# Performance work log

Measured on AMD Instinct MI355X. Metric: run time of the kernel, lower is better.

Reference implementation:

```python
import jax, jax.numpy as jnp
import numpy as np

# Model dims (match init_kwargs)
N_HEADS = 32
N_KV_HEADS = 8
DIM = 4096
HEAD_DIM = DIM // N_HEADS  # 128
N_REP = N_HEADS // N_KV_HEADS  # 4
MAX_SEQ_LEN = 2048
THETA = 10000.0


def precompute_freqs(dim, end, theta=THETA):
    inv = 1.0 / (theta ** (jnp.arange(0, dim, 2, dtype=jnp.float32) / dim))  # [dim/2]
    t = jnp.arange(end, dtype=jnp.float32)
    f = jnp.outer(t, inv)  # [end, dim/2]
    return jnp.cos(f), jnp.sin(f)


def apply_rope(x, cos, sin):
    # x: [b, s, h, d]; cos/sin: [s, d/2]. Pairs (x[...,2i], x[...,2i+1]) form complex numbers.
    xr = x[..., 0::2]
    xi = x[..., 1::2]
    c = cos[None, :, None, :]
    s = sin[None, :, None, :]
    out_r = xr * c - xi * s
    out_i = xr * s + xi * c
    return jnp.stack([out_r, out_i], axis=-1).reshape(x.shape)


def setup_inputs() -> dict:
    key = jax.random.key(0)
    ks = jax.random.split(key, 5)
    B, S = 4, 1024
    x = jax.random.normal(ks[0], (B, S, DIM), dtype=jnp.float32)
    wq = jax.random.normal(ks[1], (DIM, N_HEADS * HEAD_DIM), dtype=jnp.float32) * 0.02
    wk = jax.random.normal(ks[2], (DIM, N_KV_HEADS * HEAD_DIM), dtype=jnp.float32) * 0.02
    wv = jax.random.normal(ks[3], (DIM, N_KV_HEADS * HEAD_DIM), dtype=jnp.float32) * 0.02
    wo = jax.random.normal(ks[4], (N_HEADS * HEAD_DIM, DIM), dtype=jnp.float32) * 0.02
    # causal mask, additive: 0 on/below diagonal, -1e9 above
    mask = jnp.where(jnp.tril(jnp.ones((S, S), dtype=bool)), 0.0, -1e9).astype(jnp.float32)[None, None]
    return {"x": x, "wq": wq, "wk": wk, "wv": wv, "wo": wo, "mask": mask, "start_pos": 0}


def reference(x, wq, wk, wv, wo, mask, start_pos):
    B, S, _ = x.shape
    # QKV projections
    xq = (x @ wq).reshape(B, S, N_HEADS, HEAD_DIM)
    xk = (x @ wk).reshape(B, S, N_KV_HEADS, HEAD_DIM)
    xv = (x @ wv).reshape(B, S, N_KV_HEADS, HEAD_DIM)
    # RoPE on q, k at positions [start_pos, start_pos+S)
    cos, sin = precompute_freqs(HEAD_DIM, MAX_SEQ_LEN * 2)
    cos_s = jax.lax.dynamic_slice_in_dim(cos, start_pos, S, 0)
    sin_s = jax.lax.dynamic_slice_in_dim(sin, start_pos, S, 0)
    xq = apply_rope(xq, cos_s, sin_s)
    xk = apply_rope(xk, cos_s, sin_s)
    # KV-cache scatter-update (cache starts zeroed), then read prefix
    cache_k = jnp.zeros((B, MAX_SEQ_LEN, N_KV_HEADS, HEAD_DIM), dtype=x.dtype)
    cache_v = jnp.zeros_like(cache_k)
    cache_k = jax.lax.dynamic_update_slice(cache_k, xk, (0, start_pos, 0, 0))
    cache_v = jax.lax.dynamic_update_slice(cache_v, xv, (0, start_pos, 0, 0))
    kv_len = start_pos + S
    keys = cache_k[:, :kv_len]    # [b, kv_len, n_kv, d]
    values = cache_v[:, :kv_len]
    # GQA without materializing repeated KV: split q heads into (kv_group, rep)
    q = xq.reshape(B, S, N_KV_HEADS, N_REP, HEAD_DIM)
    scale = 1.0 / jnp.sqrt(jnp.float32(HEAD_DIM)).astype(x.dtype)
    scores = jnp.einsum('bsgrd,btgd->bgrst', q, keys) * scale  # [b, g, r, s, t]
    scores = scores + mask.reshape(1, 1, 1, S, kv_len)
    probs = jax.nn.softmax(scores, axis=-1)
    out = jnp.einsum('bgrst,btgd->bsgrd', probs, values)  # [b, s, g, r, d]
    out = out.reshape(B, S, N_HEADS * HEAD_DIM)
    return out @ wo
```

## Files before the change

kernel.cpp:

```cpp
#include <hip/hip_runtime.h>
#include <hip/hip_bf16.h>
#include <stdint.h>

typedef __bf16 bf16raw;
typedef __attribute__((ext_vector_type(8))) __bf16 bf16x8;
typedef __attribute__((ext_vector_type(4))) float f32x4;

#define DIMD 4096
#define NHEAD 32
#define NKVH 8
#define HD 128
#define SEQ 1024
#define NB 4
#define NTOK 4096
#define NQKV 6144

__device__ __forceinline__ void gload_lds16(const void* gsrc, void* ldst) {
  __builtin_amdgcn_global_load_lds(
      (const __attribute__((address_space(1))) void*)gsrc,
      (__attribute__((address_space(3))) void*)ldst, 16, 0, 0);
}

__global__ void cast_f32_bf16_kernel(const float* __restrict__ src,
                                     __hip_bfloat16* __restrict__ dst, int n) {
  int i = (blockIdx.x * 256 + threadIdx.x) * 8;
  if (i >= n) return;
  f32x4 a = *(const f32x4*)(src + i);
  f32x4 b = *(const f32x4*)(src + i + 4);
  union { bf16x8 v; __hip_bfloat16 e[8]; } o;
#pragma unroll
  for (int j = 0; j < 4; ++j) {
    o.e[j] = __float2bfloat16(a[j]);
    o.e[4 + j] = __float2bfloat16(b[j]);
  }
  *(bf16x8*)(dst + i) = o.v;
}

__global__ void transpose_qkv_kernel(const float* __restrict__ wq,
                                     const float* __restrict__ wk,
                                     const float* __restrict__ wv,
                                     __hip_bfloat16* __restrict__ dst) {
  __shared__ float tile[32][33];
  int n0 = blockIdx.x * 32;
  int k0 = blockIdx.y * 32;
  const float* src;
  int scol, nsw;
  if (n0 < 4096) { src = wq; scol = n0; nsw = 4096; }
  else if (n0 < 5120) { src = wk; scol = n0 - 4096; nsw = 1024; }
  else { src = wv; scol = n0 - 5120; nsw = 1024; }
  int tx = threadIdx.x, ty = threadIdx.y;
#pragma unroll
  for (int i = 0; i < 4; ++i)
    tile[ty + 8 * i][tx] = src[(size_t)(k0 + ty + 8 * i) * nsw + scol + tx];
  __syncthreads();
  union { ushort4 u; __hip_bfloat16 e[4]; } pk;
#pragma unroll
  for (int jj = 0; jj < 4; ++jj)
    pk.e[jj] = __float2bfloat16(tile[ty * 4 + jj][tx]);
  *(ushort4*)(dst + (size_t)(n0 + tx) * 4096 + k0 + ty * 4) = pk.u;
}

__global__ void transpose_wo_kernel(const float* __restrict__ src,
                                    __hip_bfloat16* __restrict__ dst) {
  __shared__ float tile[32][33];
  int n0 = blockIdx.x * 32, k0 = blockIdx.y * 32;
  int tx = threadIdx.x, ty = threadIdx.y;
#pragma unroll
  for (int i = 0; i < 4; ++i)
    tile[ty + 8 * i][tx] = src[(size_t)(k0 + ty + 8 * i) * 4096 + n0 + tx];
  __syncthreads();
  union { ushort4 u; __hip_bfloat16 e[4]; } pk;
#pragma unroll
  for (int jj = 0; jj < 4; ++jj)
    pk.e[jj] = __float2bfloat16(tile[ty * 4 + jj][tx]);
  *(ushort4*)(dst + (size_t)(n0 + tx) * 4096 + k0 + ty * 4) = pk.u;
}

__global__ void rope_table_kernel(float* __restrict__ cosb, float* __restrict__ sinb) {
  int idx = blockIdx.x * 256 + threadIdx.x;
  int s = idx >> 6, j = idx & 63;
  float inv = 1.0f / powf(10000.0f, (float)(2 * j) * (1.0f / 128.0f));
  float ang = (float)s * inv;
  cosb[idx] = cosf(ang);
  sinb[idx] = sinf(ang);
}


#define LGSB()                                       \
  asm volatile("s_waitcnt lgkmcnt(0)" ::: "memory"); \
  __builtin_amdgcn_sched_barrier(0)

#define QMFMA(AFR, BFR, MB, NB)                                            \
  _Pragma("unroll") for (int mf2 = 0; mf2 < 4; ++mf2)                      \
  _Pragma("unroll") for (int nf2 = 0; nf2 < 2; ++nf2)                      \
  _Pragma("unroll") for (int kk2 = 0; kk2 < 2; ++kk2)                      \
      acc[(MB) + mf2][(NB) + nf2] = __builtin_amdgcn_mfma_f32_16x16x32_bf16( \
          AFR[mf2 * 2 + kk2], BFR[nf2 * 2 + kk2], acc[(MB) + mf2][(NB) + nf2], 0, 0, 0)

#define TILE4(BUF, ST1, ST2, ST3, ST4, VM)                        \
  {                                                               \
    _Pragma("unroll") for (int mf = 0; mf < 4; ++mf)              \
    _Pragma("unroll") for (int kk = 0; kk < 2; ++kk)              \
        alo[mf * 2 + kk] = ldsA(BUF, mf, kk);                     \
    _Pragma("unroll") for (int nf = 0; nf < 2; ++nf)              \
    _Pragma("unroll") for (int kk = 0; kk < 2; ++kk)              \
        bq[nf * 2 + kk] = ldsB(BUF, nf, kk);                      \
    ST1;                                                          \
    LGSB();                                                       \
    __builtin_amdgcn_s_setprio(1);                                \
    QMFMA(alo, bq, 0, 0);                                         \
    __builtin_amdgcn_s_setprio(0);                                \
    _Pragma("unroll") for (int mf = 0; mf < 4; ++mf)              \
    _Pragma("unroll") for (int kk = 0; kk < 2; ++kk)              \
        ahi[mf * 2 + kk] = ldsA(BUF, mf + 4, kk);                 \
    ST2;                                                          \
    LGSB();                                                       \
    __builtin_amdgcn_s_setprio(1);                                \
    QMFMA(ahi, bq, 4, 0);                                         \
    __builtin_amdgcn_s_setprio(0);                                \
    _Pragma("unroll") for (int nf = 0; nf < 2; ++nf)              \
    _Pragma("unroll") for (int kk = 0; kk < 2; ++kk)              \
        bq[nf * 2 + kk] = ldsB(BUF, nf + 2, kk);                  \
    LGSB();                                                       \
    __builtin_amdgcn_s_setprio(1);                                \
    QMFMA(alo, bq, 0, 2);                                         \
    __builtin_amdgcn_s_setprio(0);                                \
    __builtin_amdgcn_s_barrier();   \
    ST3;                                                          \
    ST4;                                                          \
    __builtin_amdgcn_s_setprio(1);                                \
    QMFMA(ahi, bq, 4, 2);                                         \
    __builtin_amdgcn_s_setprio(0);                                \
    VM;                                                           \
    __builtin_amdgcn_s_barrier();   \
  }

template <typename OutT, bool ROPE>
__global__ __launch_bounds__(512, 2) void gemm256_kernel(
    const __hip_bfloat16* __restrict__ A, const __hip_bfloat16* __restrict__ BT,
    OutT* __restrict__ C, int M, int N, int K,
    const float* __restrict__ cosb, const float* __restrict__ sinb,
    __hip_bfloat16* __restrict__ vtc) {
  __shared__ __align__(16) char lds_[131072];
  const int tid = threadIdx.x;
  const int w = tid >> 6, l = tid & 63;
  const int lr = l & 15, lk = l >> 4;
  const int wm = w >> 2, wn = w & 3;

  const int nbn = N >> 8;
  const int nwg = (M >> 8) * nbn;
  const int cpx = nwg >> 3;
  const int bid = blockIdx.x;
  const int swz = (bid & 7) * cpx + (bid >> 3);
  const int m0 = (swz / nbn) << 8;
  const int n0 = (swz % nbn) << 8;

  const size_t Kb = (size_t)K * 2;
  const char* Ab = (const char*)A + (size_t)m0 * Kb;
  const char* Bb = (const char*)BT + (size_t)n0 * Kb;
  const int srcb = ((l & 7) ^ (l >> 3)) * 16;
  const int crow = l >> 3;

  auto stageA = [&](int buf, int half, int kt) {
#pragma unroll
    for (int j = 0; j < 2; ++j) {
      int row = half * 128 + (w * 2 + j) * 8 + crow;
      gload_lds16(Ab + (size_t)row * Kb + (size_t)kt * 128 + srcb,
                  lds_ + buf * 65536 + half * 16384 + (w * 2 + j) * 1024);
    }
  };
  auto stageB = [&](int buf, int half, int kt) {
#pragma unroll
    for (int j = 0; j < 2; ++j) {
      int row = half * 128 + (w * 2 + j) * 8 + crow;
      gload_lds16(Bb + (size_t)row * Kb + (size_t)kt * 128 + srcb,
                  lds_ + buf * 65536 + 32768 + half * 16384 + (w * 2 + j) * 1024);
    }
  };
  auto ldsA = [&](int buf, int mf, int kk) {
    int rih = mf * 16 + lr;
    int cb = (kk * 64 + lk * 16) ^ ((lr & 7) << 4);
    return *(const bf16x8*)(lds_ + buf * 65536 + wm * 16384 + rih * 128 + cb);
  };
  auto ldsB = [&](int buf, int nf, int kk) {
    int rih = (wn & 1) * 64 + nf * 16 + lr;
    int cb = (kk * 64 + lk * 16) ^ ((lr & 7) << 4);
    return *(const bf16x8*)(lds_ + buf * 65536 + 32768 + (wn >> 1) * 16384 +
                            rih * 128 + cb);
  };

  f32x4 acc[8][4] = {};
  bf16x8 alo[8], ahi[8], bq[4];

  stageA(0, 0, 0);
  stageA(0, 1, 0);
  stageB(0, 0, 0);
  stageB(0, 1, 0);
  stageA(1, 0, 1);
  stageA(1, 1, 1);
  asm volatile("s_waitcnt vmcnt(4)" ::: "memory");
  __builtin_amdgcn_s_barrier();

  const int NT = K >> 6;
  for (int E = 0; E < NT - 2; E += 2) {
    TILE4(0, stageB(1, 0, E + 1), stageB(1, 1, E + 1),
          stageA(0, 0, E + 2), stageA(0, 1, E + 2),
          asm volatile("s_waitcnt vmcnt(4)" ::: "memory"));
    TILE4(1, stageB(0, 0, E + 2), stageB(0, 1, E + 2),
          stageA(1, 0, E + 3), stageA(1, 1, E + 3),
          asm volatile("s_waitcnt vmcnt(4)" ::: "memory"));
  }
  TILE4(0, stageB(1, 0, NT - 1), stageB(1, 1, NT - 1), (void)0, (void)0,
        asm volatile("s_waitcnt vmcnt(0)" ::: "memory"));
  TILE4(1, (void)0, (void)0, (void)0, (void)0, (void)0);

#pragma unroll
  for (int mf = 0; mf < 8; ++mf) {
    int row = m0 + wm * 128 + mf * 16 + lk * 4;
#pragma unroll
    for (int nf = 0; nf < 4; ++nf) {
      int colb = n0 + wn * 64 + nf * 16;
      f32x4 v = acc[mf][nf];
      if constexpr (ROPE) {
        if (colb < 5120) {
          int d = (colb & 127) + lr;
          int jj = d >> 1;
          bool even = (d & 1) == 0;
#pragma unroll
          for (int j = 0; j < 4; ++j) {
            float p = __shfl_xor(v[j], 1);
            int s = (row + j) & (SEQ - 1);
            float c = cosb[s * 64 + jj];
            float sn = sinb[s * 64 + jj];
            v[j] = even ? (v[j] * c - p * sn) : (p * sn + v[j] * c);
          }
        } else {
          int col = colb + lr;
          int d = col & 127;
          int hk = (col >> 7) & 7;
          int b = row >> 10;
          int s = row & (SEQ - 1);
          union { uint64_t u; __hip_bfloat16 e[4]; } pk;
#pragma unroll
          for (int j = 0; j < 4; ++j) pk.e[j] = __float2bfloat16(v[j]);
          size_t off = ((size_t)((b * 8 + hk) * 16 + (s >> 6)) * 128 + d) * 64 +
                       (s & 63);
          *(uint64_t*)(vtc + off) = pk.u;
          continue;
        }
      }
#pragma unroll
      for (int j = 0; j < 4; ++j) {
        size_t off = (size_t)(row + j) * N + colb + lr;
        if constexpr (sizeof(OutT) == 2)
          C[off] = __float2bfloat16(v[j]);
        else
          C[off] = v[j];
      }
    }
  }
}

__global__ __launch_bounds__(512, 2) void attn_kernel(
    const __hip_bfloat16* __restrict__ qkv,
    const __hip_bfloat16* __restrict__ vtc,
    __hip_bfloat16* __restrict__ out) {
  __shared__ __align__(16) char Ks[2][16384];
  __shared__ __align__(16) char Vs[2][16384];
  __shared__ __align__(16) char Ps[8][4096];

  const int tid = threadIdx.x;
  const int w = tid >> 6, l = tid & 63;
  const int lr = l & 15, lk = l >> 4;
  const int bx = blockIdx.x;
  const int p = bx >> 5;
  const int bh = bx & 31;
  const int b = bh >> 3;
  const int hk = bh & 7;
  const int h = hk * 4 + (w & 3);
  const int qh = w >> 2;

  const char* KgB = (const char*)qkv +
                    ((size_t)(b * SEQ) * NQKV + DIMD + hk * HD) * 2;
  const char* VgB = (const char*)vtc + (size_t)(b * NKVH + hk) * (16 * 16384);
  char* Pw = &Ps[w][0];

  const float cs = 0.12752039889171495f;
  const float ebias = 11.541560327111707f;

  auto stageK = [&](int buf, int kvb) {
#pragma unroll
    for (int j = 0; j < 2; ++j) {
      int i2 = w * 2 + j;
      int row = i2 * 4 + (l >> 4);
      int si = ((l & 15) * 16) ^ ((row & 7) << 4);
      gload_lds16(KgB + (size_t)(kvb + row) * (NQKV * 2) + si,
                  &Ks[buf][i2 * 1024]);
    }
  };
  auto stageV = [&](int buf, int t) {
#pragma unroll
    for (int j = 0; j < 2; ++j) {
      int i2 = w * 2 + j;
      int row = i2 * 8 + (l >> 3);
      int si = ((l & 7) * 16) ^ ((row & 7) << 4);
      gload_lds16(VgB + (size_t)t * 16384 + row * 128 + si,
                  &Vs[buf][i2 * 1024]);
    }
  };

  for (int qsel = 0; qsel < 2; ++qsel) {
    const int qtile = qsel ? (15 - p) : p;
    const int qbaseW = qtile * 64 + qh * 32;
    const int nkv = qtile + 1;

    bf16x8 aq[8];
#pragma unroll
    for (int qg = 0; qg < 2; ++qg) {
      const __hip_bfloat16* Qp =
          qkv + (size_t)(b * SEQ + qbaseW + qg * 16 + lr) * NQKV + h * HD + lk * 8;
#pragma unroll
      for (int ks = 0; ks < 4; ++ks) aq[qg * 4 + ks] = *(const bf16x8*)(Qp + ks * 32);
    }

    f32x4 O[16] = {};
    float lsum[8] = {0.f, 0.f, 0.f, 0.f, 0.f, 0.f, 0.f, 0.f};

    stageK(0, 0);
    stageV(0, 0);
    asm volatile("s_waitcnt vmcnt(0)" ::: "memory");
    __syncthreads();

    for (int t = 0; t < nkv; ++t) {
      const int cur = t & 1;
      if (t + 1 < nkv) {
        stageK(cur ^ 1, (t + 1) * 64);
        stageV(cur ^ 1, t + 1);
      }
      const int kvb = t * 64;

      f32x4 st[8] = {};
      __builtin_amdgcn_s_setprio(1);
#pragma unroll
      for (int nt = 0; nt < 4; ++nt) {
        int row = nt * 16 + lr;
        const char* kr = &Ks[cur][row * 256];
        int sw = (row & 7) << 4;
        bf16x8 bk[4];
#pragma unroll
        for (int ks = 0; ks < 4; ++ks)
          bk[ks] = *(const bf16x8*)(kr + ((ks * 64 + lk * 16) ^ sw));
#pragma unroll
        for (int qg = 0; qg < 2; ++qg)
#pragma unroll
          for (int ks = 0; ks < 4; ++ks)
            st[qg * 4 + nt] = __builtin_amdgcn_mfma_f32_16x16x32_bf16(
                aq[qg * 4 + ks], bk[ks], st[qg * 4 + nt], 0, 0, 0);
      }
      __builtin_amdgcn_s_setprio(0);

#pragma unroll
      for (int qg = 0; qg < 2; ++qg) {
        const bool needmask = (kvb + 63 > qbaseW + qg * 16);
#pragma unroll
        for (int j = 0; j < 4; ++j) {
          int qrow = qbaseW + qg * 16 + lk * 4 + j;
          int prow = lk * 4 + j;
          int sw = (prow & 7) << 4;
#pragma unroll
          for (int nt = 0; nt < 4; ++nt) {
            float pv = exp2f(fmaf(st[qg * 4 + nt][j], cs, -ebias));
            if (needmask && (kvb + nt * 16 + lr > qrow)) pv = 0.f;
            lsum[qg * 4 + j] += pv;
            *(__hip_bfloat16*)(Pw + qg * 2048 + prow * 128 +
                               (((nt * 16 + lr) * 2) ^ sw)) = __float2bfloat16(pv);
          }
        }
      }

      asm volatile("s_waitcnt lgkmcnt(0)" ::: "memory");
      __builtin_amdgcn_sched_barrier(0);

      __builtin_amdgcn_s_setprio(1);
#pragma unroll
      for (int ks = 0; ks < 2; ++ks) {
        bf16x8 ap[2];
#pragma unroll
        for (int qg = 0; qg < 2; ++qg)
          ap[qg] = *(const bf16x8*)(Pw + qg * 2048 + lr * 128 +
                                    ((ks * 64 + lk * 16) ^ ((lr & 7) << 4)));
#pragma unroll
        for (int dt = 0; dt < 8; ++dt) {
          int row = dt * 16 + lr;
          bf16x8 bv = *(const bf16x8*)(&Vs[cur][row * 128 +
                                               ((ks * 64 + lk * 16) ^ ((row & 7) << 4))]);
#pragma unroll
          for (int qg = 0; qg < 2; ++qg)
            O[qg * 8 + dt] = __builtin_amdgcn_mfma_f32_16x16x32_bf16(
                ap[qg], bv, O[qg * 8 + dt], 0, 0, 0);
        }
      }
      __builtin_amdgcn_s_setprio(0);

      __syncthreads();
    }

#pragma unroll
    for (int qg = 0; qg < 2; ++qg) {
#pragma unroll
      for (int j = 0; j < 4; ++j) {
        float rs = lsum[qg * 4 + j];
        rs += __shfl_xor(rs, 1);
        rs += __shfl_xor(rs, 2);
        rs += __shfl_xor(rs, 4);
        rs += __shfl_xor(rs, 8);
        float inv = 1.0f / rs;
        __hip_bfloat16* orow =
            out + (size_t)(b * SEQ + qbaseW + qg * 16 + lk * 4 + j) * DIMD + h * HD;
#pragma unroll
        for (int dt = 0; dt < 8; ++dt)
          orow[dt * 16 + lr] = __float2bfloat16(O[qg * 8 + dt][j] * inv);
      }
    }
  }
}

extern "C" void kernel_launch(void* const* d_in, const int* in_sizes, int n_in,
                              void* d_out, int out_size, void* d_ws, size_t ws_size,
                              hipStream_t stream) {
  const float* x = (const float*)d_in[0];
  const float* wq = (const float*)d_in[1];
  const float* wk = (const float*)d_in[2];
  const float* wv = (const float*)d_in[3];
  const float* wo = (const float*)d_in[4];
  float* out = (float*)d_out;

  char* ws = (char*)d_ws;
  const size_t MB = 1024 * 1024;
  __hip_bfloat16* xb = (__hip_bfloat16*)(ws);
  __hip_bfloat16* wqkvt = (__hip_bfloat16*)(ws + 32 * MB);
  __hip_bfloat16* wot = (__hip_bfloat16*)(ws + 80 * MB);
  __hip_bfloat16* qkv = (__hip_bfloat16*)(ws + 112 * MB);
  __hip_bfloat16* vtc = (__hip_bfloat16*)(ws + 160 * MB);
  float* cosb = (float*)(ws + 168 * MB);
  float* sinb = cosb + SEQ * 64;

  cast_f32_bf16_kernel<<<NTOK * DIMD / 8 / 256, 256, 0, stream>>>(x, xb, NTOK * DIMD);
  transpose_qkv_kernel<<<dim3(192, 128), dim3(32, 8), 0, stream>>>(wq, wk, wv, wqkvt);
  transpose_wo_kernel<<<dim3(128, 128), dim3(32, 8), 0, stream>>>(wo, wot);
  rope_table_kernel<<<SEQ * 64 / 256, 256, 0, stream>>>(cosb, sinb);
  gemm256_kernel<__hip_bfloat16, true><<<dim3(384), 512, 0, stream>>>(
      xb, wqkvt, qkv, NTOK, NQKV, DIMD, cosb, sinb, vtc);
  attn_kernel<<<dim3(256), 512, 0, stream>>>(qkv, vtc, xb);
  gemm256_kernel<float, false><<<dim3(256), 512, 0, stream>>>(
      xb, wot, out, NTOK, DIMD, DIMD, nullptr, nullptr, nullptr);
}
```

Baseline: 468.7 us.

## Simplify GEMM pipeline to plain double buffering with full-tile prefetch

Replaces the staggered A/B staging schedule (A prefetched two tiles ahead, B one tile ahead, split across four points inside the tile) with simple double buffering. Each step now issues the whole next A and B tile at the start of the compute step, then waits for all loads (vmcnt(0)) before a single barrier. This cuts a barrier per tile and simplifies scheduling. The cost is a shallower prefetch and an exposed full drain of outstanding loads each iteration, so memory latency may be hidden less well.

```diff
diff --git a/kernel.cpp b/kernel.cpp
--- a/kernel.cpp
+++ b/kernel.cpp
@@ -97,15 +97,15 @@
       acc[(MB) + mf2][(NB) + nf2] = __builtin_amdgcn_mfma_f32_16x16x32_bf16( \
           AFR[mf2 * 2 + kk2], BFR[nf2 * 2 + kk2], acc[(MB) + mf2][(NB) + nf2], 0, 0, 0)
 
-#define TILE4(BUF, ST1, ST2, ST3, ST4, VM)                        \
+#define TILE1(BUF, ST)                                            \
   {                                                               \
+    ST;                                                           \
     _Pragma("unroll") for (int mf = 0; mf < 4; ++mf)              \
     _Pragma("unroll") for (int kk = 0; kk < 2; ++kk)              \
         alo[mf * 2 + kk] = ldsA(BUF, mf, kk);                     \
     _Pragma("unroll") for (int nf = 0; nf < 2; ++nf)              \
     _Pragma("unroll") for (int kk = 0; kk < 2; ++kk)              \
         bq[nf * 2 + kk] = ldsB(BUF, nf, kk);                      \
-    ST1;                                                          \
     LGSB();                                                       \
     __builtin_amdgcn_s_setprio(1);                                \
     QMFMA(alo, bq, 0, 0);                                         \
@@ -113,7 +113,6 @@
     _Pragma("unroll") for (int mf = 0; mf < 4; ++mf)              \
     _Pragma("unroll") for (int kk = 0; kk < 2; ++kk)              \
         ahi[mf * 2 + kk] = ldsA(BUF, mf + 4, kk);                 \
-    ST2;                                                          \
     LGSB();                                                       \
     __builtin_amdgcn_s_setprio(1);                                \
     QMFMA(ahi, bq, 4, 0);                                         \
@@ -125,14 +124,11 @@
     __builtin_amdgcn_s_setprio(1);                                \
     QMFMA(alo, bq, 0, 2);                                         \
     __builtin_amdgcn_s_setprio(0);                                \
-    __builtin_amdgcn_s_barrier();   \
-    ST3;                                                          \
-    ST4;                                                          \
     __builtin_amdgcn_s_setprio(1);                                \
     QMFMA(ahi, bq, 4, 2);                                         \
     __builtin_amdgcn_s_setprio(0);                                \
-    VM;                                                           \
-    __builtin_amdgcn_s_barrier();   \
+    asm volatile("s_waitcnt vmcnt(0)" ::: "memory");              \
+    __builtin_amdgcn_s_barrier();    \
   }
 
 template <typename OutT, bool ROPE>
@@ -161,21 +157,25 @@
   const int srcb = ((l & 7) ^ (l >> 3)) * 16;
   const int crow = l >> 3;
 
-  auto stageA = [&](int buf, int half, int kt) {
-#pragma unroll
-    for (int j = 0; j < 2; ++j) {
-      int row = half * 128 + (w * 2 + j) * 8 + crow;
-      gload_lds16(Ab + (size_t)row * Kb + (size_t)kt * 128 + srcb,
-                  lds_ + buf * 65536 + half * 16384 + (w * 2 + j) * 1024);
-    }
-  };
-  auto stageB = [&](int buf, int half, int kt) {
-#pragma unroll
-    for (int j = 0; j < 2; ++j) {
-      int row = half * 128 + (w * 2 + j) * 8 + crow;
-      gload_lds16(Bb + (size_t)row * Kb + (size_t)kt * 128 + srcb,
-                  lds_ + buf * 65536 + 32768 + half * 16384 + (w * 2 + j) * 1024);
-    }
+  auto stageA = [&](int buf, int kt) {
+#pragma unroll
+    for (int hf = 0; hf < 2; ++hf)
+#pragma unroll
+      for (int j = 0; j < 2; ++j) {
+        int row = hf * 128 + (w * 2 + j) * 8 + crow;
+        gload_lds16(Ab + (size_t)row * Kb + (size_t)kt * 128 + srcb,
+                    lds_ + buf * 65536 + hf * 16384 + (w * 2 + j) * 1024);
+      }
+  };
+  auto stageB = [&](int buf, int kt) {
+#pragma unroll
+    for (int hf = 0; hf < 2; ++hf)
+#pragma unroll
+      for (int j = 0; j < 2; ++j) {
+        int row = hf * 128 + (w * 2 + j) * 8 + crow;
+        gload_lds16(Bb + (size_t)row * Kb + (size_t)kt * 128 + srcb,
+                    lds_ + buf * 65536 + 32768 + hf * 16384 + (w * 2 + j) * 1024);
+      }
   };
   auto ldsA = [&](int buf, int mf, int kk) {
     int rih = mf * 16 + lr;
@@ -192,27 +192,18 @@
   f32x4 acc[8][4] = {};
   bf16x8 alo[8], ahi[8], bq[4];
 
-  stageA(0, 0, 0);
-  stageA(0, 1, 0);
-  stageB(0, 0, 0);
-  stageB(0, 1, 0);
-  stageA(1, 0, 1);
-  stageA(1, 1, 1);
-  asm volatile("s_waitcnt vmcnt(4)" ::: "memory");
+  stageA(0, 0);
+  stageB(0, 0);
+  asm volatile("s_waitcnt vmcnt(0)" ::: "memory");
   __builtin_amdgcn_s_barrier();
 
   const int NT = K >> 6;
   for (int E = 0; E < NT - 2; E += 2) {
-    TILE4(0, stageB(1, 0, E + 1), stageB(1, 1, E + 1),
-          stageA(0, 0, E + 2), stageA(0, 1, E + 2),
-          asm volatile("s_waitcnt vmcnt(4)" ::: "memory"));
-    TILE4(1, stageB(0, 0, E + 2), stageB(0, 1, E + 2),
-          stageA(1, 0, E + 3), stageA(1, 1, E + 3),
-          asm volatile("s_waitcnt vmcnt(4)" ::: "memory"));
+    TILE1(0, (stageA(1, E + 1), stageB(1, E + 1)));
+    TILE1(1, (stageA(0, E + 2), stageB(0, E + 2)));
   }
-  TILE4(0, stageB(1, 0, NT - 1), stageB(1, 1, NT - 1), (void)0, (void)0,
-        asm volatile("s_waitcnt vmcnt(0)" ::: "memory"));
-  TILE4(1, (void)0, (void)0, (void)0, (void)0, (void)0);
+  TILE1(0, (stageA(1, NT - 1), stageB(1, NT - 1)));
+  TILE1(1, (void)0);
 
 #pragma unroll
   for (int mf = 0; mf < 8; ++mf) {
```

After: 491.4 us. 4.9% more time.
